# Kernel optimization log

Hardware: AMD Instinct MI355X
Metric: run time of the kernel (lower is better)

Reference implementation:

```python
import jax, jax.numpy as jnp
import numpy as np

NUM_TOKENS = 2048
HIDDEN = 1024
INTER = 2048
NUM_EXPERTS = 8
TOPK = 2


def setup_inputs() -> dict:
    key = jax.random.key(0)
    k1, k2, k3, k4 = jax.random.split(key, 4)
    hidden_states = jax.random.normal(k1, (NUM_TOKENS, HIDDEN), dtype=jnp.float32)
    router_logits = jax.random.normal(k2, (NUM_TOKENS, NUM_EXPERTS), dtype=jnp.float32)
    # fc1: [E, hidden, 2*intermediate] (proj/gate for SwiGLU), fc2: [E, intermediate, hidden]
    w1 = jax.random.normal(k3, (NUM_EXPERTS, HIDDEN, 2 * INTER), dtype=jnp.float32) * 0.02
    w2 = jax.random.normal(k4, (NUM_EXPERTS, INTER, HIDDEN), dtype=jnp.float32) * 0.02
    return {"hidden_states": hidden_states, "router_logits": router_logits, "w1": w1, "w2": w2}


def _grouped_gemm(x, w, expert_ids):
    """x: [T, D], w: [E, D, O], expert_ids: [T] -> [T, O].
    Tokens are routed to expert expert_ids[t]; equivalent to the sequential
    per-expert GEMM on contiguously sorted tokens. Small fixed loop over E."""
    out = jnp.zeros((x.shape[0], w.shape[-1]), dtype=x.dtype)
    for e in range(w.shape[0]):
        mask = (expert_ids == e)[:, None]
        out = out + jnp.where(mask, x, 0.0) @ w[e]
    return out


def reference(hidden_states, router_logits, w1, w2):
    # top-k routing + softmax over the selected logits
    top_logits, top_idx = jax.lax.top_k(router_logits, TOPK)      # [N, K]
    scores = jax.nn.softmax(top_logits, axis=-1)                  # [N, K]

    flat_idx = top_idx.reshape(-1)                                # [N*K]
    sorted_indices = jnp.argsort(flat_idx)                        # permute tokens grouped by expert
    permuted = hidden_states[sorted_indices // TOPK]              # [N*K, D]
    sorted_experts = flat_idx[sorted_indices]                     # [N*K] expert id per permuted row

    fc1_out = _grouped_gemm(permuted, w1, sorted_experts)         # [N*K, 2*I]
    proj, gate = jnp.split(fc1_out, 2, axis=-1)
    act = jax.nn.silu(proj) * gate                                # SwiGLU
    expert_out = _grouped_gemm(act, w2, sorted_experts)           # [N*K, D]

    # unpermute (scatter back) and weighted combine over top-k
    unpermuted = jnp.zeros_like(expert_out).at[sorted_indices].set(expert_out)
    unpermuted = unpermuted.reshape(-1, TOPK, expert_out.shape[-1])
    return (unpermuted * scores[..., None]).sum(axis=1)           # [N, D]
```

## Files before the change

### kernel.cpp

```cpp
#include <hip/hip_runtime.h>
#include <hip/hip_bf16.h>

constexpr int T = 2048;
constexpr int H = 1024;
constexpr int I = 2048;
constexpr int N2 = 2 * I;
constexpr int RCAP = 5120;
constexpr int MAXT = 40;

constexpr int WS_OFF = 16;
constexpr int WS_TEXP = 32;
constexpr int WS_TOPKP = 4256;
constexpr int WS_ROWTOK = 8352;
constexpr int WS_TOKROW = 13472;
constexpr size_t WSB_ZROW = 114688;
constexpr size_t WSB_HSB  = 131072;
constexpr size_t WSB_ACT  = 8u << 20;
constexpr size_t WSB_PW1  = 32u << 20;
constexpr size_t WSB_PW2  = 96u << 20;

constexpr int W1T_BLKS = 8 * 32 * 8;
constexpr int W2T_BLKS = 8 * 64 * 2;
constexpr int HSB_BLKS = T * H / 2048;
constexpr int FC1_BLKS = 32 * MAXT;

typedef __attribute__((ext_vector_type(4))) float f32x4;
typedef __attribute__((ext_vector_type(8))) short s16x8;

__device__ __forceinline__ short f2bf(float f) {
    unsigned u = __float_as_uint(f);
    u += 0x7FFFu + ((u >> 16) & 1u);
    return (short)(u >> 16);
}

#define MFMA16(a, b, c) __builtin_amdgcn_mfma_f32_16x16x32_bf16(a, b, c, 0, 0, 0)

__device__ __forceinline__ void gl2lds16(const void* g, void* l) {
    __builtin_amdgcn_global_load_lds(
        (const __attribute__((address_space(1))) void*)g,
        (__attribute__((address_space(3))) void*)l, 16, 0, 0);
}

__global__ __launch_bounds__(256) void routing_kernel(const float* __restrict__ logits,
                                                      int* __restrict__ wsi,
                                                      float* __restrict__ wsf) {
    __shared__ int cnt[8], base[9], fill[8];
    const int t = threadIdx.x;
    if (t < 8) { cnt[t] = 0; fill[t] = 0; }
    for (int r = t; r < RCAP; r += 256) wsi[WS_ROWTOK + r] = -1;
    unsigned short* zr = (unsigned short*)((char*)wsi + WSB_ZROW);
    for (int i = t; i < H; i += 256) zr[i] = 0;
    __syncthreads();

    int e0a[8], e1a[8];
    #pragma unroll
    for (int j = 0; j < 8; j++) {
        int tok = t * 8 + j;
        const float* l = logits + tok * 8;
        float v0 = -1e30f; int i0 = 0;
        #pragma unroll
        for (int i = 0; i < 8; i++) { float v = l[i]; if (v > v0) { v0 = v; i0 = i; } }
        float v1 = -1e30f; int i1 = 0;
        #pragma unroll
        for (int i = 0; i < 8; i++) { if (i == i0) continue; float v = l[i]; if (v > v1) { v1 = v; i1 = i; } }
        float ex = __expf(v1 - v0);
        float inv = 1.f / (1.f + ex);
        wsf[WS_TOPKP + tok * 2] = inv;
        wsf[WS_TOPKP + tok * 2 + 1] = ex * inv;
        e0a[j] = i0; e1a[j] = i1;
        atomicAdd(&cnt[i0], 1);
        atomicAdd(&cnt[i1], 1);
    }
    __syncthreads();
    if (t == 0) {
        int acc = 0;
        for (int e = 0; e < 8; e++) { base[e] = acc; acc += (cnt[e] + 127) & ~127; }
        base[8] = acc;
        for (int e = 0; e < 9; e++) wsi[WS_OFF + e] = base[e];
    }
    __syncthreads();
    for (int tt = t; tt < MAXT; tt += 256) {
        int rb = tt * 128, ex = 0;
        for (int e = 0; e < 8; e++)
            if (rb >= base[e] && rb < base[e + 1]) ex = e;
        wsi[WS_TEXP + tt] = ex;
    }
    #pragma unroll
    for (int j = 0; j < 8; j++) {
        int tok = t * 8 + j;
        int ee[2] = {e0a[j], e1a[j]};
        #pragma unroll
        for (int k = 0; k < 2; k++) {
            int e = ee[k];
            int slot = atomicAdd(&fill[e], 1);
            int r = base[e] + slot;
            wsi[WS_ROWTOK + r] = tok;
            wsi[WS_TOKROW + tok * 2 + k] = r;
        }
    }
}

__global__ __launch_bounds__(256) void prep_kernel(
    const float* __restrict__ w1, unsigned short* __restrict__ pw1,
    const float* __restrict__ w2, unsigned short* __restrict__ pw2,
    const float* __restrict__ hs, unsigned short* __restrict__ hsb) {
    __shared__ __align__(16) unsigned short L[32 * 512];
    const int t = threadIdx.x;
    if (blockIdx.x < W1T_BLKS) {
        int b = blockIdx.x;
        int cs = b & 7, k0i = (b >> 3) & 31, e = b >> 8;
        const float* src = w1 + (size_t)e * H * N2 + (size_t)(k0i * 32) * N2 + cs * 512;
        #pragma unroll
        for (int i = 0; i < 8; i++) {
            int c = t + i * 256;
            int row = c >> 6, col8 = (c & 63) * 8;
            const float* sp = src + (size_t)row * N2 + col8;
            f32x4 a = *(const f32x4*)sp;
            f32x4 bb = *(const f32x4*)(sp + 4);
            s16x8 s = {f2bf(a[0]), f2bf(a[1]), f2bf(a[2]), f2bf(a[3]),
                       f2bf(bb[0]), f2bf(bb[1]), f2bf(bb[2]), f2bf(bb[3])};
            *(s16x8*)&L[c * 8] = s;
        }
        __syncthreads();
        int gate = cs >> 2;
        int ctbase = (cs & 3) * 8;
        unsigned short* dstb = pw1 + (size_t)(e * 1024 + k0i) * 4096;
        #pragma unroll
        for (int i = 0; i < 8; i++) {
            int cidx = t + i * 256;
            int within = cidx & 31, nhalf = (cidx >> 5) & 1;
            int kg = (cidx >> 6) & 3, ctp = cidx >> 8;
            int x = ctp * 64 + nhalf * 32 + within;
            int n = gate * 32 + nhalf * 64 + within;
            s16x8 s;
            #pragma unroll
            for (int kk = 0; kk < 8; kk++) s[kk] = (short)L[(kg * 8 + kk) * 512 + x];
            int ct = ctbase + ctp;
            *(s16x8*)(dstb + (size_t)ct * 32 * 4096 + (kg * 128 + n) * 8) = s;
        }
    } else if (blockIdx.x < W1T_BLKS + W2T_BLKS) {
        int b = blockIdx.x - W1T_BLKS;
        int cs = b & 1, k0i = (b >> 1) & 63, e = b >> 7;
        const float* src = w2 + (size_t)e * I * H + (size_t)(k0i * 32) * H + cs * 512;
        #pragma unroll
        for (int i = 0; i < 8; i++) {
            int c = t + i * 256;
            int row = c >> 6, col8 = (c & 63) * 8;
            const float* sp = src + (size_t)row * H + col8;
            f32x4 a = *(const f32x4*)sp;
            f32x4 bb = *(const f32x4*)(sp + 4);
            s16x8 s = {f2bf(a[0]), f2bf(a[1]), f2bf(a[2]), f2bf(a[3]),
                       f2bf(bb[0]), f2bf(bb[1]), f2bf(bb[2]), f2bf(bb[3])};
            *(s16x8*)&L[c * 8] = s;
        }
        __syncthreads();
        unsigned short* dstb = pw2 + (size_t)(e * 512 + k0i) * 4096;
        #pragma unroll
        for (int i = 0; i < 8; i++) {
            int cidx = t + i * 256;
            int n = cidx & 127, kg = (cidx >> 7) & 3, htp = cidx >> 9;
            int x = htp * 128 + n;
            s16x8 s;
            #pragma unroll
            for (int kk = 0; kk < 8; kk++) s[kk] = (short)L[(kg * 8 + kk) * 512 + x];
            int ht = cs * 4 + htp;
            *(s16x8*)(dstb + (size_t)ht * 64 * 4096 + (kg * 128 + n) * 8) = s;
        }
    } else {
        int i = ((blockIdx.x - W1T_BLKS - W2T_BLKS) * 256 + t) * 8;
        f32x4 a = *(const f32x4*)(hs + i);
        f32x4 b = *(const f32x4*)(hs + i + 4);
        s16x8 s = {f2bf(a[0]), f2bf(a[1]), f2bf(a[2]), f2bf(a[3]),
                   f2bf(b[0]), f2bf(b[1]), f2bf(b[2]), f2bf(b[3])};
        *(s16x8*)(hsb + i) = s;
    }
}

__global__ __launch_bounds__(256, 2) void fc1_kernel(
    const unsigned short* __restrict__ hsb, const unsigned short* __restrict__ pw1,
    const int* __restrict__ wsi, const unsigned short* __restrict__ zrow,
    unsigned short* __restrict__ act) {
    __shared__ __align__(16) unsigned short Al[512 * 8];
    __shared__ __align__(16) unsigned short Bl[512 * 8];
    const int t = threadIdx.x;
    const int ct = blockIdx.x & 31, rt = blockIdx.x >> 5;
    const int rowb = rt * 128;
    if (rowb >= wsi[WS_OFF + 8]) return;
    const int e = wsi[WS_TEXP + rt];
    const unsigned short* pb = pw1 + (size_t)((e * 32 + ct) * 32) * 4096;

    const int m = t & 127;
    const int tok = wsi[WS_ROWTOK + rowb + m];
    const unsigned short* rp = (tok >= 0) ? (hsb + (size_t)tok * H) : zrow;
    const int kga = t >> 7;

    const int lane = t & 63, w = t >> 6, wr = w >> 1, wc = w & 1;
    const int q = lane >> 4, l16 = lane & 15;

    f32x4 zero = {0.f, 0.f, 0.f, 0.f};
    f32x4 acc[4][4];
    #pragma unroll
    for (int mi = 0; mi < 4; mi++)
        #pragma unroll
        for (int ni = 0; ni < 4; ni++) acc[mi][ni] = zero;

    for (int k0i = 0; k0i < 32; k0i++) {
        const int k0 = k0i * 32;
        gl2lds16(rp + k0 + kga * 8, &Al[t * 8]);
        gl2lds16(rp + k0 + (kga + 2) * 8, &Al[(t + 256) * 8]);
        const unsigned short* ps = pb + (size_t)k0i * 4096;
        gl2lds16(ps + t * 8, &Bl[t * 8]);
        gl2lds16(ps + (t + 256) * 8, &Bl[(t + 256) * 8]);
        __syncthreads();

        s16x8 af[4], bf[4];
        #pragma unroll
        for (int mi = 0; mi < 4; mi++)
            af[mi] = *(const s16x8*)&Al[(q * 128 + wr * 64 + mi * 16 + l16) * 8];
        #pragma unroll
        for (int ni = 0; ni < 4; ni++)
            bf[ni] = *(const s16x8*)&Bl[(q * 128 + wc * 64 + ni * 16 + l16) * 8];
        #pragma unroll
        for (int mi = 0; mi < 4; mi++)
            #pragma unroll
            for (int ni = 0; ni < 4; ni++)
                acc[mi][ni] = MFMA16(af[mi], bf[ni], acc[mi][ni]);
        __syncthreads();
    }

    #pragma unroll
    for (int mi = 0; mi < 4; mi++)
        #pragma unroll
        for (int r = 0; r < 4; r++) {
            int row = rowb + wr * 64 + mi * 16 + q * 4 + r;
            #pragma unroll
            for (int ni = 0; ni < 2; ni++) {
                int col = ct * 64 + wc * 32 + ni * 16 + l16;
                float p = acc[mi][ni][r], g = acc[mi][ni + 2][r];
                float val = p * g / (1.f + __expf(-p));
                act[(size_t)row * I + col] = (unsigned short)f2bf(val);
            }
        }
}

__global__ __launch_bounds__(256, 2) void fc2_kernel(
    const unsigned short* __restrict__ act, const unsigned short* __restrict__ pw2,
    const int* __restrict__ wsi, float* __restrict__ eo) {
    __shared__ __align__(16) unsigned short Al[512 * 8];
    __shared__ __align__(16) unsigned short Bl[512 * 8];
    const int t = threadIdx.x;
    const int ht = blockIdx.x, rt = blockIdx.y, ks = blockIdx.z;
    const int rowb = rt * 128;
    if (rowb >= wsi[WS_OFF + 8]) return;
    const int e = wsi[WS_TEXP + rt];
    const unsigned short* pb = pw2 + (size_t)((e * 8 + ht) * 64) * 4096;

    const int m = t & 127;
    const unsigned short* rp = act + (size_t)(rowb + m) * I;
    const int kga = t >> 7;

    const int lane = t & 63, w = t >> 6, wr = w >> 1, wc = w & 1;
    const int q = lane >> 4, l16 = lane & 15;

    f32x4 zero = {0.f, 0.f, 0.f, 0.f};
    f32x4 acc[4][4];
    #pragma unroll
    for (int mi = 0; mi < 4; mi++)
        #pragma unroll
        for (int ni = 0; ni < 4; ni++) acc[mi][ni] = zero;

    for (int k0i = ks * 32; k0i < ks * 32 + 32; k0i++) {
        const int k0 = k0i * 32;
        gl2lds16(rp + k0 + kga * 8, &Al[t * 8]);
        gl2lds16(rp + k0 + (kga + 2) * 8, &Al[(t + 256) * 8]);
        const unsigned short* ps = pb + (size_t)k0i * 4096;
        gl2lds16(ps + t * 8, &Bl[t * 8]);
        gl2lds16(ps + (t + 256) * 8, &Bl[(t + 256) * 8]);
        __syncthreads();

        s16x8 af[4], bf[4];
        #pragma unroll
        for (int mi = 0; mi < 4; mi++)
            af[mi] = *(const s16x8*)&Al[(q * 128 + wr * 64 + mi * 16 + l16) * 8];
        #pragma unroll
        for (int ni = 0; ni < 4; ni++)
            bf[ni] = *(const s16x8*)&Bl[(q * 128 + wc * 64 + ni * 16 + l16) * 8];
        #pragma unroll
        for (int mi = 0; mi < 4; mi++)
            #pragma unroll
            for (int ni = 0; ni < 4; ni++)
                acc[mi][ni] = MFMA16(af[mi], bf[ni], acc[mi][ni]);
        __syncthreads();
    }

    float* ed = eo + (size_t)ks * RCAP * H;
    #pragma unroll
    for (int mi = 0; mi < 4; mi++)
        #pragma unroll
        for (int r = 0; r < 4; r++) {
            int row = rowb + wr * 64 + mi * 16 + q * 4 + r;
            #pragma unroll
            for (int ni = 0; ni < 4; ni++) {
                int col = ht * 128 + wc * 64 + ni * 16 + l16;
                ed[(size_t)row * H + col] = acc[mi][ni][r];
            }
        }
}

__global__ __launch_bounds__(256) void combine_kernel(
    const float* __restrict__ eo, const int* __restrict__ wsi,
    const float* __restrict__ wsf, float* __restrict__ out) {
    const int tok = blockIdx.x;
    const int r0 = wsi[WS_TOKROW + tok * 2], r1 = wsi[WS_TOKROW + tok * 2 + 1];
    const float s0 = wsf[WS_TOPKP + tok * 2], s1 = wsf[WS_TOPKP + tok * 2 + 1];
    const float* a0 = eo + (size_t)r0 * H;
    const float* a1 = eo + (size_t)RCAP * H + (size_t)r0 * H;
    const float* b0 = eo + (size_t)r1 * H;
    const float* b1 = eo + (size_t)RCAP * H + (size_t)r1 * H;
    const int c = threadIdx.x * 4;
    f32x4 va0 = *(const f32x4*)(a0 + c), va1 = *(const f32x4*)(a1 + c);
    f32x4 vb0 = *(const f32x4*)(b0 + c), vb1 = *(const f32x4*)(b1 + c);
    f32x4 r;
    #pragma unroll
    for (int i = 0; i < 4; i++) r[i] = s0 * (va0[i] + va1[i]) + s1 * (vb0[i] + vb1[i]);
    *(f32x4*)(out + (size_t)tok * H + c) = r;
}

extern "C" void kernel_launch(void* const* d_in, const int* in_sizes, int n_in,
                              void* d_out, int out_size, void* d_ws, size_t ws_size,
                              hipStream_t stream) {
    const float* hs     = (const float*)d_in[0];
    const float* logits = (const float*)d_in[1];
    const float* w1     = (const float*)d_in[2];
    const float* w2     = (const float*)d_in[3];
    float* out = (float*)d_out;
    int* wsi = (int*)d_ws;
    float* wsf = (float*)d_ws;
    unsigned short* zrow = (unsigned short*)((char*)d_ws + WSB_ZROW);
    unsigned short* hsb  = (unsigned short*)((char*)d_ws + WSB_HSB);
    unsigned short* act  = (unsigned short*)((char*)d_ws + WSB_ACT);
    unsigned short* pw1  = (unsigned short*)((char*)d_ws + WSB_PW1);
    unsigned short* pw2  = (unsigned short*)((char*)d_ws + WSB_PW2);
    float* eo = (float*)((char*)d_ws + WSB_PW1);

    routing_kernel<<<1, 256, 0, stream>>>(logits, wsi, wsf);
    prep_kernel<<<W1T_BLKS + W2T_BLKS + HSB_BLKS, 256, 0, stream>>>(w1, pw1, w2, pw2, hs, hsb);
    fc1_kernel<<<FC1_BLKS, 256, 0, stream>>>(hsb, pw1, wsi, zrow, act);
    fc2_kernel<<<dim3(8, MAXT, 2), 256, 0, stream>>>(act, pw2, wsi, eo);
    combine_kernel<<<T, 256, 0, stream>>>(eo, wsi, wsf, out);
}
```

Measured before the change: 382.8 us.

## Overlap w2 conversion with fc1 and hs conversion with routing

Result: faster. 372.1 us (-2.8%).

```diff
diff --git a/kernel.cpp b/kernel.cpp
--- a/kernel.cpp
+++ b/kernel.cpp
@@ -41,11 +41,22 @@
         (__attribute__((address_space(3))) void*)l, 16, 0, 0);
 }
 
-__global__ __launch_bounds__(256) void routing_kernel(const float* __restrict__ logits,
-                                                      int* __restrict__ wsi,
-                                                      float* __restrict__ wsf) {
+__global__ __launch_bounds__(256) void routing_hs_kernel(const float* __restrict__ logits,
+                                                         int* __restrict__ wsi,
+                                                         float* __restrict__ wsf,
+                                                         const float* __restrict__ hs,
+                                                         unsigned short* __restrict__ hsb) {
+    const int t = threadIdx.x;
+    if (blockIdx.x > 0) {
+        int i = (((int)blockIdx.x - 1) * 256 + t) * 8;
+        f32x4 a = *(const f32x4*)(hs + i);
+        f32x4 b = *(const f32x4*)(hs + i + 4);
+        s16x8 s = {f2bf(a[0]), f2bf(a[1]), f2bf(a[2]), f2bf(a[3]),
+                   f2bf(b[0]), f2bf(b[1]), f2bf(b[2]), f2bf(b[3])};
+        *(s16x8*)(hsb + i) = s;
+        return;
+    }
     __shared__ int cnt[8], base[9], fill[8];
-    const int t = threadIdx.x;
     if (t < 8) { cnt[t] = 0; fill[t] = 0; }
     for (int r = t; r < RCAP; r += 256) wsi[WS_ROWTOK + r] = -1;
     unsigned short* zr = (unsigned short*)((char*)wsi + WSB_ZROW);
@@ -100,46 +111,53 @@
     }
 }
 
-__global__ __launch_bounds__(256) void prep_kernel(
-    const float* __restrict__ w1, unsigned short* __restrict__ pw1,
-    const float* __restrict__ w2, unsigned short* __restrict__ pw2,
-    const float* __restrict__ hs, unsigned short* __restrict__ hsb) {
+__global__ __launch_bounds__(256) void prep_w1_kernel(
+    const float* __restrict__ w1, unsigned short* __restrict__ pw1) {
     __shared__ __align__(16) unsigned short L[32 * 512];
     const int t = threadIdx.x;
-    if (blockIdx.x < W1T_BLKS) {
-        int b = blockIdx.x;
-        int cs = b & 7, k0i = (b >> 3) & 31, e = b >> 8;
-        const float* src = w1 + (size_t)e * H * N2 + (size_t)(k0i * 32) * N2 + cs * 512;
-        #pragma unroll
-        for (int i = 0; i < 8; i++) {
-            int c = t + i * 256;
-            int row = c >> 6, col8 = (c & 63) * 8;
-            const float* sp = src + (size_t)row * N2 + col8;
-            f32x4 a = *(const f32x4*)sp;
-            f32x4 bb = *(const f32x4*)(sp + 4);
-            s16x8 s = {f2bf(a[0]), f2bf(a[1]), f2bf(a[2]), f2bf(a[3]),
-                       f2bf(bb[0]), f2bf(bb[1]), f2bf(bb[2]), f2bf(bb[3])};
-            *(s16x8*)&L[c * 8] = s;
-        }
-        __syncthreads();
-        int gate = cs >> 2;
-        int ctbase = (cs & 3) * 8;
-        unsigned short* dstb = pw1 + (size_t)(e * 1024 + k0i) * 4096;
-        #pragma unroll
-        for (int i = 0; i < 8; i++) {
-            int cidx = t + i * 256;
-            int within = cidx & 31, nhalf = (cidx >> 5) & 1;
-            int kg = (cidx >> 6) & 3, ctp = cidx >> 8;
-            int x = ctp * 64 + nhalf * 32 + within;
-            int n = gate * 32 + nhalf * 64 + within;
-            s16x8 s;
-            #pragma unroll
-            for (int kk = 0; kk < 8; kk++) s[kk] = (short)L[(kg * 8 + kk) * 512 + x];
-            int ct = ctbase + ctp;
-            *(s16x8*)(dstb + (size_t)ct * 32 * 4096 + (kg * 128 + n) * 8) = s;
-        }
-    } else if (blockIdx.x < W1T_BLKS + W2T_BLKS) {
-        int b = blockIdx.x - W1T_BLKS;
+    int b = blockIdx.x;
+    int cs = b & 7, k0i = (b >> 3) & 31, e = b >> 8;
+    const float* src = w1 + (size_t)e * H * N2 + (size_t)(k0i * 32) * N2 + cs * 512;
+    #pragma unroll
+    for (int i = 0; i < 8; i++) {
+        int c = t + i * 256;
+        int row = c >> 6, col8 = (c & 63) * 8;
+        const float* sp = src + (size_t)row * N2 + col8;
+        f32x4 a = *(const f32x4*)sp;
+        f32x4 bb = *(const f32x4*)(sp + 4);
+        s16x8 s = {f2bf(a[0]), f2bf(a[1]), f2bf(a[2]), f2bf(a[3]),
+                   f2bf(bb[0]), f2bf(bb[1]), f2bf(bb[2]), f2bf(bb[3])};
+        *(s16x8*)&L[c * 8] = s;
+    }
+    __syncthreads();
+    int gate = cs >> 2;
+    int ctbase = (cs & 3) * 8;
+    unsigned short* dstb = pw1 + (size_t)(e * 1024 + k0i) * 4096;
+    #pragma unroll
+    for (int i = 0; i < 8; i++) {
+        int cidx = t + i * 256;
+        int within = cidx & 31, nhalf = (cidx >> 5) & 1;
+        int kg = (cidx >> 6) & 3, ctp = cidx >> 8;
+        int x = ctp * 64 + nhalf * 32 + within;
+        int n = gate * 32 + nhalf * 64 + within;
+        s16x8 s;
+        #pragma unroll
+        for (int kk = 0; kk < 8; kk++) s[kk] = (short)L[(kg * 8 + kk) * 512 + x];
+        int ct = ctbase + ctp;
+        *(s16x8*)(dstb + (size_t)ct * 32 * 4096 + (kg * 128 + n) * 8) = s;
+    }
+}
+
+__global__ __launch_bounds__(256, 2) void fc1_kernel(
+    const unsigned short* __restrict__ hsb, const unsigned short* __restrict__ pw1,
+    const int* __restrict__ wsi, const unsigned short* __restrict__ zrow,
+    unsigned short* __restrict__ act,
+    const float* __restrict__ w2, unsigned short* __restrict__ pw2) {
+    __shared__ __align__(16) unsigned short SM[32 * 512];
+    const int t = threadIdx.x;
+
+    if (blockIdx.x >= FC1_BLKS) {
+        int b = (int)blockIdx.x - FC1_BLKS;
         int cs = b & 1, k0i = (b >> 1) & 63, e = b >> 7;
         const float* src = w2 + (size_t)e * I * H + (size_t)(k0i * 32) * H + cs * 512;
         #pragma unroll
@@ -151,7 +169,7 @@
             f32x4 bb = *(const f32x4*)(sp + 4);
             s16x8 s = {f2bf(a[0]), f2bf(a[1]), f2bf(a[2]), f2bf(a[3]),
                        f2bf(bb[0]), f2bf(bb[1]), f2bf(bb[2]), f2bf(bb[3])};
-            *(s16x8*)&L[c * 8] = s;
+            *(s16x8*)&SM[c * 8] = s;
         }
         __syncthreads();
         unsigned short* dstb = pw2 + (size_t)(e * 512 + k0i) * 4096;
@@ -162,27 +180,15 @@
             int x = htp * 128 + n;
             s16x8 s;
             #pragma unroll
-            for (int kk = 0; kk < 8; kk++) s[kk] = (short)L[(kg * 8 + kk) * 512 + x];
+            for (int kk = 0; kk < 8; kk++) s[kk] = (short)SM[(kg * 8 + kk) * 512 + x];
             int ht = cs * 4 + htp;
             *(s16x8*)(dstb + (size_t)ht * 64 * 4096 + (kg * 128 + n) * 8) = s;
         }
-    } else {
-        int i = ((blockIdx.x - W1T_BLKS - W2T_BLKS) * 256 + t) * 8;
-        f32x4 a = *(const f32x4*)(hs + i);
-        f32x4 b = *(const f32x4*)(hs + i + 4);
-        s16x8 s = {f2bf(a[0]), f2bf(a[1]), f2bf(a[2]), f2bf(a[3]),
-                   f2bf(b[0]), f2bf(b[1]), f2bf(b[2]), f2bf(b[3])};
-        *(s16x8*)(hsb + i) = s;
-    }
-}
-
-__global__ __launch_bounds__(256, 2) void fc1_kernel(
-    const unsigned short* __restrict__ hsb, const unsigned short* __restrict__ pw1,
-    const int* __restrict__ wsi, const unsigned short* __restrict__ zrow,
-    unsigned short* __restrict__ act) {
-    __shared__ __align__(16) unsigned short Al[512 * 8];
-    __shared__ __align__(16) unsigned short Bl[512 * 8];
-    const int t = threadIdx.x;
+        return;
+    }
+
+    unsigned short* Al = SM;
+    unsigned short* Bl = SM + 4096;
     const int ct = blockIdx.x & 31, rt = blockIdx.x >> 5;
     const int rowb = rt * 128;
     if (rowb >= wsi[WS_OFF + 8]) return;
@@ -343,9 +349,9 @@
     unsigned short* pw2  = (unsigned short*)((char*)d_ws + WSB_PW2);
     float* eo = (float*)((char*)d_ws + WSB_PW1);
 
-    routing_kernel<<<1, 256, 0, stream>>>(logits, wsi, wsf);
-    prep_kernel<<<W1T_BLKS + W2T_BLKS + HSB_BLKS, 256, 0, stream>>>(w1, pw1, w2, pw2, hs, hsb);
-    fc1_kernel<<<FC1_BLKS, 256, 0, stream>>>(hsb, pw1, wsi, zrow, act);
+    routing_hs_kernel<<<1 + HSB_BLKS, 256, 0, stream>>>(logits, wsi, wsf, hs, hsb);
+    prep_w1_kernel<<<W1T_BLKS, 256, 0, stream>>>(w1, pw1);
+    fc1_kernel<<<FC1_BLKS + W2T_BLKS, 256, 0, stream>>>(hsb, pw1, wsi, zrow, act, w2, pw2);
     fc2_kernel<<<dim3(8, MAXT, 2), 256, 0, stream>>>(act, pw2, wsi, eo);
     combine_kernel<<<T, 256, 0, stream>>>(eo, wsi, wsf, out);
 }
```
